# Kernel optimization log

Hardware: AMD Instinct MI355X
Metric: run time of the kernel (lower is better)

## Reference

```python
import jax, jax.numpy as jnp
import numpy as np

N_NODES = 50000
N_EDGES = 625000
D_IN, D_HID, D_OUT = 512, 128, 1


def gcn_conv(x, W, b, src, dst, n_nodes):
    """PyG GCNConv: add self-loops, symmetric D^-1/2 (A+I) D^-1/2 normalization.
    x: [N, d_in], W: [d_in, d_out], b: [d_out], src/dst: [E] int.
    """
    xw = x @ W  # [N, d_out] - linear before propagation (PyG order)
    # degree including self-loop
    deg = jax.ops.segment_sum(jnp.ones_like(src, dtype=xw.dtype), dst,
                              num_segments=n_nodes) + 1.0
    dinv = jax.lax.rsqrt(deg)  # [N]
    norm = dinv[src] * dinv[dst]  # [E]
    # neighbor aggregation (scatter-add over destination nodes)
    agg = jax.ops.segment_sum(xw[src] * norm[:, None], dst, num_segments=n_nodes)
    # self-loop contribution: norm_ii = dinv_i^2
    agg = agg + xw * (dinv * dinv)[:, None]
    return agg + b


def layer_norm(x, gamma, beta, eps=1e-5):
    mu = jnp.mean(x, axis=-1, keepdims=True)
    var = jnp.var(x, axis=-1, keepdims=True)
    return (x - mu) * jax.lax.rsqrt(var + eps) * gamma + beta


def setup_inputs() -> dict:
    key = jax.random.key(0)
    ks = jax.random.split(key, 12)
    x = jax.random.normal(ks[0], (N_NODES, D_IN), dtype=jnp.float32)
    edge_index = jax.random.randint(ks[1], (2, N_EDGES), 0, N_NODES, dtype=jnp.int64)

    def glorot(k, shape):
        lim = np.sqrt(6.0 / (shape[0] + shape[1]))
        return jax.random.uniform(k, shape, jnp.float32, -lim, lim)

    return {
        "x": x,
        "W1": glorot(ks[2], (D_IN, D_HID)), "b1": jnp.zeros((D_HID,), jnp.float32),
        "gamma1": jnp.ones((D_HID,), jnp.float32), "beta1": jnp.zeros((D_HID,), jnp.float32),
        "W2": glorot(ks[3], (D_HID, D_HID)), "b2": jnp.zeros((D_HID,), jnp.float32),
        "W3": glorot(ks[4], (D_HID, D_HID)), "b3": jnp.zeros((D_HID,), jnp.float32),
        "W4": glorot(ks[5], (D_HID, D_OUT)), "b4": jnp.zeros((D_OUT,), jnp.float32),
        "edge_index": edge_index,
    }


def reference(x, W1, b1, gamma1, beta1, W2, b2, W3, b3, W4, b4, edge_index):
    # eval mode: F.dropout(training=False) is identity
    src, dst = edge_index[0], edge_index[1]
    n = x.shape[0]
    h = jax.nn.relu(layer_norm(gcn_conv(x, W1, b1, src, dst, n), gamma1, beta1))
    h = jax.nn.relu(gcn_conv(h, W2, b2, src, dst, n))
    h = jax.nn.relu(gcn_conv(h, W3, b3, src, dst, n))
    h = gcn_conv(h, W4, b4, src, dst, n)
    return jnp.squeeze(h, axis=-1)  # [N]
```

## Files before the change

### kernel.cpp

```cpp
#include <hip/hip_runtime.h>
#include <hip/hip_bf16.h>
#include <cstdint>

#define D_IN 512
#define D_HID 128

typedef unsigned short u16;
typedef __attribute__((ext_vector_type(8))) short short8;
typedef __attribute__((ext_vector_type(4))) float f32x4;

__device__ __forceinline__ u16 f2bf(float f) {
    unsigned u = __float_as_uint(f);
    u = (u + 0x7FFFu + ((u >> 16) & 1u)) >> 16;
    return (u16)u;
}
__device__ __forceinline__ float bf_lo(unsigned u) { return __uint_as_float(u << 16); }
__device__ __forceinline__ float bf_hi(unsigned u) { return __uint_as_float(u & 0xFFFF0000u); }

__global__ __launch_bounds__(256) void k_deg_int(const int* __restrict__ dst,
                                                 int* __restrict__ deg, int E) {
    int e = blockIdx.x * 256 + threadIdx.x;
    if (e < E) atomicAdd(&deg[dst[e]], 1);
}

__global__ __launch_bounds__(256) void k_scan_block(const int* __restrict__ deg,
                                                    int* __restrict__ rowptr,
                                                    int* __restrict__ bsum, int N) {
    __shared__ int sh[256];
    int i = blockIdx.x * 256 + threadIdx.x;
    int v = (i < N) ? deg[i] : 0;
    sh[threadIdx.x] = v;
    __syncthreads();
#pragma unroll
    for (int off = 1; off < 256; off <<= 1) {
        int t = (threadIdx.x >= off) ? sh[threadIdx.x - off] : 0;
        __syncthreads();
        sh[threadIdx.x] += t;
        __syncthreads();
    }
    int incl = sh[threadIdx.x];
    if (i < N) rowptr[i] = incl - v;
    if (threadIdx.x == 255) bsum[blockIdx.x] = incl;
}

__global__ __launch_bounds__(256) void k_scan_partials(int* __restrict__ bsum, int P) {
    __shared__ int sh[256];
    int v = (threadIdx.x < P) ? bsum[threadIdx.x] : 0;
    sh[threadIdx.x] = v;
    __syncthreads();
#pragma unroll
    for (int off = 1; off < 256; off <<= 1) {
        int t = (threadIdx.x >= off) ? sh[threadIdx.x - off] : 0;
        __syncthreads();
        sh[threadIdx.x] += t;
        __syncthreads();
    }
    if (threadIdx.x < P) bsum[threadIdx.x] = sh[threadIdx.x] - v;
}

__global__ __launch_bounds__(256) void k_apply_offset(int* __restrict__ rowptr,
                                                      const int* __restrict__ bsum,
                                                      int* __restrict__ deg_cursor,
                                                      float* __restrict__ dinv,
                                                      int N, int E) {
    int i = blockIdx.x * 256 + threadIdx.x;
    if (i == 0) rowptr[N] = E;
    if (i >= N) return;
    int dv = deg_cursor[i];
    int rp = rowptr[i] + bsum[i >> 8];
    rowptr[i] = rp;
    deg_cursor[i] = rp;
    dinv[i] = rsqrtf((float)dv + 1.0f);
}

__global__ __launch_bounds__(256) void k_fill_csr(const int* __restrict__ src,
                                                  const int* __restrict__ dst,
                                                  int* __restrict__ cursor,
                                                  int* __restrict__ csr, int E) {
    int e = blockIdx.x * 256 + threadIdx.x;
    if (e >= E) return;
    int pos = atomicAdd(&cursor[dst[e]], 1);
    csr[pos] = src[e];
}

__global__ __launch_bounds__(256) void k_wt(const float* __restrict__ W,
                                            u16* __restrict__ WT, int K) {
    int t = blockIdx.x * 256 + threadIdx.x;
    if (t >= 128 * K) return;
    int c = t / K, k = t - c * K;
    WT[t] = f2bf(W[(size_t)k * 128 + c]);
}

template <int K>
__global__ __launch_bounds__(256) void k_gemm_mfma(const float* __restrict__ X,
                                                   const u16* __restrict__ WT,
                                                   u16* __restrict__ Y, int N) {
    __shared__ u16 Xs[64 * 40];
    __shared__ u16 Ws[128 * 40];
    const int tid = threadIdx.x;
    const int wv = tid >> 6;
    const int lane = tid & 63;
    const int row0 = blockIdx.x * 64;
    const int rsel = lane & 15;
    const int kgrp = (lane >> 4) * 8;

    f32x4 acc[8];
#pragma unroll
    for (int c = 0; c < 8; ++c) acc[c] = (f32x4){0.f, 0.f, 0.f, 0.f};

    for (int k0 = 0; k0 < K; k0 += 32) {
        {
            int r = tid >> 2;
            int kk = (tid & 3) * 8;
            int row = row0 + r;
            float v[8];
            if (row < N) {
                float4 p0 = *(const float4*)&X[(size_t)row * K + k0 + kk];
                float4 p1 = *(const float4*)&X[(size_t)row * K + k0 + kk + 4];
                v[0] = p0.x; v[1] = p0.y; v[2] = p0.z; v[3] = p0.w;
                v[4] = p1.x; v[5] = p1.y; v[6] = p1.z; v[7] = p1.w;
            } else {
#pragma unroll
                for (int i = 0; i < 8; ++i) v[i] = 0.f;
            }
            union { u16 us[8]; short8 v8; } tmp;
#pragma unroll
            for (int i = 0; i < 8; ++i) tmp.us[i] = f2bf(v[i]);
            *(short8*)&Xs[r * 40 + kk] = tmp.v8;
        }
        {
            int col = tid >> 1;
            int kh = (tid & 1) * 16;
            const u16* g = &WT[(size_t)col * K + k0 + kh];
            u16* d = &Ws[col * 40 + kh];
            *(short8*)d = *(const short8*)g;
            *(short8*)(d + 8) = *(const short8*)(g + 8);
        }
        __syncthreads();
        short8 a = *(const short8*)&Xs[(wv * 16 + rsel) * 40 + kgrp];
#pragma unroll
        for (int c = 0; c < 8; ++c) {
            short8 b = *(const short8*)&Ws[(c * 16 + rsel) * 40 + kgrp];
            acc[c] = __builtin_amdgcn_mfma_f32_16x16x32_bf16(a, b, acc[c], 0, 0, 0);
        }
        __syncthreads();
    }
#pragma unroll
    for (int r = 0; r < 4; ++r) {
        int row = row0 + wv * 16 + (lane >> 4) * 4 + r;
        if (row < N) {
#pragma unroll
            for (int c = 0; c < 8; ++c)
                Y[(size_t)row * 128 + c * 16 + rsel] = f2bf(acc[c][r]);
        }
    }
}

__global__ __launch_bounds__(256) void k_gather_ln_relu(const u16* __restrict__ XW,
                                                        const int* __restrict__ rowptr,
                                                        const int* __restrict__ csr,
                                                        const float* __restrict__ dinv,
                                                        const float* __restrict__ b,
                                                        const float* __restrict__ gamma,
                                                        const float* __restrict__ beta,
                                                        float* __restrict__ H, int N) {
    int node = blockIdx.x * 4 + (threadIdx.x >> 6);
    int lane = threadIdx.x & 63;
    if (node >= N) return;
    float di = dinv[node];
    int beg = rowptr[node], end = rowptr[node + 1];
    const int loff = 2 * lane;
    float a0 = 0.f, a1 = 0.f;
    int j = beg;
    for (; j + 3 < end; j += 4) {
        int s0 = csr[j], s1 = csr[j + 1], s2 = csr[j + 2], s3 = csr[j + 3];
        float w0 = dinv[s0], w1 = dinv[s1], w2 = dinv[s2], w3 = dinv[s3];
        unsigned u0 = *(const unsigned*)&XW[(size_t)s0 * 128 + loff];
        unsigned u1 = *(const unsigned*)&XW[(size_t)s1 * 128 + loff];
        unsigned u2 = *(const unsigned*)&XW[(size_t)s2 * 128 + loff];
        unsigned u3 = *(const unsigned*)&XW[(size_t)s3 * 128 + loff];
        a0 += bf_lo(u0) * w0 + bf_lo(u1) * w1 + bf_lo(u2) * w2 + bf_lo(u3) * w3;
        a1 += bf_hi(u0) * w0 + bf_hi(u1) * w1 + bf_hi(u2) * w2 + bf_hi(u3) * w3;
    }
    for (; j < end; ++j) {
        int s = csr[j];
        float w = dinv[s];
        unsigned u = *(const unsigned*)&XW[(size_t)s * 128 + loff];
        a0 += bf_lo(u) * w;
        a1 += bf_hi(u) * w;
    }
    unsigned us = *(const unsigned*)&XW[(size_t)node * 128 + loff];
    float d2 = di * di;
    float2 bb = *(const float2*)&b[loff];
    float v0 = a0 * di + bf_lo(us) * d2 + bb.x;
    float v1 = a1 * di + bf_hi(us) * d2 + bb.y;
    float s = v0 + v1;
    float sq = v0 * v0 + v1 * v1;
#pragma unroll
    for (int off = 32; off; off >>= 1) {
        s  += __shfl_xor(s, off);
        sq += __shfl_xor(sq, off);
    }
    float mu  = s * (1.f / 128.f);
    float var = sq * (1.f / 128.f) - mu * mu;
    float rr  = rsqrtf(var + 1e-5f);
    float2 gg = *(const float2*)&gamma[loff];
    float2 be = *(const float2*)&beta[loff];
    float o0 = fmaxf((v0 - mu) * rr * gg.x + be.x, 0.f);
    float o1 = fmaxf((v1 - mu) * rr * gg.y + be.y, 0.f);
    *(float2*)&H[(size_t)node * 128 + loff] = make_float2(o0, o1);
}

__global__ __launch_bounds__(256) void k_gather_relu(const u16* __restrict__ XW,
                                                     const int* __restrict__ rowptr,
                                                     const int* __restrict__ csr,
                                                     const float* __restrict__ dinv,
                                                     const float* __restrict__ b,
                                                     float* __restrict__ H, int N) {
    int node = blockIdx.x * 4 + (threadIdx.x >> 6);
    int lane = threadIdx.x & 63;
    if (node >= N) return;
    float di = dinv[node];
    int beg = rowptr[node], end = rowptr[node + 1];
    const int loff = 2 * lane;
    float a0 = 0.f, a1 = 0.f;
    int j = beg;
    for (; j + 3 < end; j += 4) {
        int s0 = csr[j], s1 = csr[j + 1], s2 = csr[j + 2], s3 = csr[j + 3];
        float w0 = dinv[s0], w1 = dinv[s1], w2 = dinv[s2], w3 = dinv[s3];
        unsigned u0 = *(const unsigned*)&XW[(size_t)s0 * 128 + loff];
        unsigned u1 = *(const unsigned*)&XW[(size_t)s1 * 128 + loff];
        unsigned u2 = *(const unsigned*)&XW[(size_t)s2 * 128 + loff];
        unsigned u3 = *(const unsigned*)&XW[(size_t)s3 * 128 + loff];
        a0 += bf_lo(u0) * w0 + bf_lo(u1) * w1 + bf_lo(u2) * w2 + bf_lo(u3) * w3;
        a1 += bf_hi(u0) * w0 + bf_hi(u1) * w1 + bf_hi(u2) * w2 + bf_hi(u3) * w3;
    }
    for (; j < end; ++j) {
        int s = csr[j];
        float w = dinv[s];
        unsigned u = *(const unsigned*)&XW[(size_t)s * 128 + loff];
        a0 += bf_lo(u) * w;
        a1 += bf_hi(u) * w;
    }
    unsigned us = *(const unsigned*)&XW[(size_t)node * 128 + loff];
    float d2 = di * di;
    float2 bb = *(const float2*)&b[loff];
    float v0 = fmaxf(a0 * di + bf_lo(us) * d2 + bb.x, 0.f);
    float v1 = fmaxf(a1 * di + bf_hi(us) * d2 + bb.y, 0.f);
    *(float2*)&H[(size_t)node * 128 + loff] = make_float2(v0, v1);
}

__global__ __launch_bounds__(256) void k_gather_dot(const u16* __restrict__ XW,
                                                    const int* __restrict__ rowptr,
                                                    const int* __restrict__ csr,
                                                    const float* __restrict__ dinv,
                                                    const float* __restrict__ b,
                                                    const float* __restrict__ W4,
                                                    float* __restrict__ XW4, int N) {
    int node = blockIdx.x * 4 + (threadIdx.x >> 6);
    int lane = threadIdx.x & 63;
    if (node >= N) return;
    float di = dinv[node];
    int beg = rowptr[node], end = rowptr[node + 1];
    const int loff = 2 * lane;
    float a0 = 0.f, a1 = 0.f;
    int j = beg;
    for (; j + 3 < end; j += 4) {
        int s0 = csr[j], s1 = csr[j + 1], s2 = csr[j + 2], s3 = csr[j + 3];
        float w0 = dinv[s0], w1 = dinv[s1], w2 = dinv[s2], w3 = dinv[s3];
        unsigned u0 = *(const unsigned*)&XW[(size_t)s0 * 128 + loff];
        unsigned u1 = *(const unsigned*)&XW[(size_t)s1 * 128 + loff];
        unsigned u2 = *(const unsigned*)&XW[(size_t)s2 * 128 + loff];
        unsigned u3 = *(const unsigned*)&XW[(size_t)s3 * 128 + loff];
        a0 += bf_lo(u0) * w0 + bf_lo(u1) * w1 + bf_lo(u2) * w2 + bf_lo(u3) * w3;
        a1 += bf_hi(u0) * w0 + bf_hi(u1) * w1 + bf_hi(u2) * w2 + bf_hi(u3) * w3;
    }
    for (; j < end; ++j) {
        int s = csr[j];
        float w = dinv[s];
        unsigned u = *(const unsigned*)&XW[(size_t)s * 128 + loff];
        a0 += bf_lo(u) * w;
        a1 += bf_hi(u) * w;
    }
    unsigned us = *(const unsigned*)&XW[(size_t)node * 128 + loff];
    float d2 = di * di;
    float2 bb = *(const float2*)&b[loff];
    float v0 = fmaxf(a0 * di + bf_lo(us) * d2 + bb.x, 0.f);
    float v1 = fmaxf(a1 * di + bf_hi(us) * d2 + bb.y, 0.f);
    float2 w4v = *(const float2*)&W4[loff];
    float t = v0 * w4v.x + v1 * w4v.y;
#pragma unroll
    for (int off = 32; off; off >>= 1) t += __shfl_xor(t, off);
    if (lane == 0) XW4[node] = t;
}

__global__ __launch_bounds__(256) void k_final_scalar(const float* __restrict__ XW4,
                                                      const int* __restrict__ rowptr,
                                                      const int* __restrict__ csr,
                                                      const float* __restrict__ dinv,
                                                      const float* __restrict__ b4,
                                                      float* __restrict__ OUT, int N) {
    int i = blockIdx.x * 256 + threadIdx.x;
    if (i >= N) return;
    float di = dinv[i];
    int beg = rowptr[i], end = rowptr[i + 1];
    float acc = 0.f;
    for (int j = beg; j < end; ++j) {
        int s = csr[j];
        acc += XW4[s] * dinv[s];
    }
    OUT[i] = acc * di + XW4[i] * di * di + b4[0];
}

static inline size_t alignup(size_t x) { return (x + 255) & ~(size_t)255; }

extern "C" void kernel_launch(void* const* d_in, const int* in_sizes, int n_in,
                              void* d_out, int out_size, void* d_ws, size_t ws_size,
                              hipStream_t stream) {
    const float* x      = (const float*)d_in[0];
    const float* W1     = (const float*)d_in[1];
    const float* b1     = (const float*)d_in[2];
    const float* gamma1 = (const float*)d_in[3];
    const float* beta1  = (const float*)d_in[4];
    const float* W2     = (const float*)d_in[5];
    const float* b2     = (const float*)d_in[6];
    const float* W3     = (const float*)d_in[7];
    const float* b3     = (const float*)d_in[8];
    const float* W4     = (const float*)d_in[9];
    const float* b4     = (const float*)d_in[10];
    const int*   ei     = (const int*)d_in[11];

    const int N = in_sizes[0] / D_IN;
    const int E = in_sizes[11] / 2;
    const int* src = ei;
    const int* dst = ei + E;

    char* ws = (char*)d_ws;
    size_t off = 0;
    int*   deg_cur = (int*)(ws + off);   off += alignup((size_t)N * 4);
    int*   rowptr  = (int*)(ws + off);   off += alignup((size_t)(N + 1) * 4);
    int*   bsum    = (int*)(ws + off);   off += alignup(256 * 4);
    float* dinv    = (float*)(ws + off); off += alignup((size_t)N * 4);
    float* xw4     = (float*)(ws + off); off += alignup((size_t)N * 4);
    int*   csr     = (int*)(ws + off);   off += alignup((size_t)E * 4);
    u16*   WT1     = (u16*)(ws + off);   off += alignup((size_t)128 * 512 * 2);
    u16*   WT2     = (u16*)(ws + off);   off += alignup((size_t)128 * 128 * 2);
    u16*   WT3     = (u16*)(ws + off);   off += alignup((size_t)128 * 128 * 2);
    u16*   XW      = (u16*)(ws + off);   off += alignup((size_t)N * 128 * 2);
    float* H       = (float*)(ws + off);

    const int scanBlocks = (N + 255) / 256;

    hipMemsetAsync(deg_cur, 0, (size_t)N * 4, stream);
    k_deg_int<<<(E + 255) / 256, 256, 0, stream>>>(dst, deg_cur, E);
    k_scan_block<<<scanBlocks, 256, 0, stream>>>(deg_cur, rowptr, bsum, N);
    k_scan_partials<<<1, 256, 0, stream>>>(bsum, scanBlocks);
    k_apply_offset<<<scanBlocks, 256, 0, stream>>>(rowptr, bsum, deg_cur, dinv, N, E);
    k_fill_csr<<<(E + 255) / 256, 256, 0, stream>>>(src, dst, deg_cur, csr, E);

    k_wt<<<(128 * 512 + 255) / 256, 256, 0, stream>>>(W1, WT1, 512);
    k_wt<<<(128 * 128 + 255) / 256, 256, 0, stream>>>(W2, WT2, 128);
    k_wt<<<(128 * 128 + 255) / 256, 256, 0, stream>>>(W3, WT3, 128);

    const int gemmGrid   = (N + 63) / 64;
    const int gatherGrid = (N + 3) / 4;

    k_gemm_mfma<512><<<gemmGrid, 256, 0, stream>>>(x, WT1, XW, N);
    k_gather_ln_relu<<<gatherGrid, 256, 0, stream>>>(XW, rowptr, csr, dinv,
                                                     b1, gamma1, beta1, H, N);
    k_gemm_mfma<128><<<gemmGrid, 256, 0, stream>>>(H, WT2, XW, N);
    k_gather_relu<<<gatherGrid, 256, 0, stream>>>(XW, rowptr, csr, dinv, b2, H, N);
    k_gemm_mfma<128><<<gemmGrid, 256, 0, stream>>>(H, WT3, XW, N);
    k_gather_dot<<<gatherGrid, 256, 0, stream>>>(XW, rowptr, csr, dinv, b3, W4, xw4, N);
    k_final_scalar<<<(N + 255) / 256, 256, 0, stream>>>(xw4, rowptr, csr, dinv,
                                                        b4, (float*)d_out, N);
}
```

Before: 399.0 us.

## Store hidden activations in bf16, widen gather loads, parallelize final aggregation

```diff
diff --git a/kernel.cpp b/kernel.cpp
--- a/kernel.cpp
+++ b/kernel.cpp
@@ -6,16 +6,18 @@
 #define D_HID 128
 
 typedef unsigned short u16;
+typedef unsigned int u32;
 typedef __attribute__((ext_vector_type(8))) short short8;
 typedef __attribute__((ext_vector_type(4))) float f32x4;
 
 __device__ __forceinline__ u16 f2bf(float f) {
-    unsigned u = __float_as_uint(f);
+    u32 u = __float_as_uint(f);
     u = (u + 0x7FFFu + ((u >> 16) & 1u)) >> 16;
     return (u16)u;
 }
-__device__ __forceinline__ float bf_lo(unsigned u) { return __uint_as_float(u << 16); }
-__device__ __forceinline__ float bf_hi(unsigned u) { return __uint_as_float(u & 0xFFFF0000u); }
+__device__ __forceinline__ float bfc(short x) {
+    return __uint_as_float(((u32)(u16)x) << 16);
+}
 
 __global__ __launch_bounds__(256) void k_deg_int(const int* __restrict__ dst,
                                                  int* __restrict__ deg, int E) {
@@ -83,16 +85,29 @@
     csr[pos] = src[e];
 }
 
-__global__ __launch_bounds__(256) void k_wt(const float* __restrict__ W,
-                                            u16* __restrict__ WT, int K) {
+__global__ __launch_bounds__(256) void k_wt_all(const float* __restrict__ W1,
+                                                const float* __restrict__ W2,
+                                                const float* __restrict__ W3,
+                                                u16* __restrict__ WT1,
+                                                u16* __restrict__ WT2,
+                                                u16* __restrict__ WT3) {
     int t = blockIdx.x * 256 + threadIdx.x;
-    if (t >= 128 * K) return;
-    int c = t / K, k = t - c * K;
-    WT[t] = f2bf(W[(size_t)k * 128 + c]);
-}
-
-template <int K>
-__global__ __launch_bounds__(256) void k_gemm_mfma(const float* __restrict__ X,
+    if (t < 65536) {
+        int c = t >> 9, k = t & 511;
+        WT1[t] = f2bf(W1[(size_t)k * 128 + c]);
+    } else if (t < 65536 + 16384) {
+        int u = t - 65536;
+        int c = u >> 7, k = u & 127;
+        WT2[u] = f2bf(W2[(size_t)k * 128 + c]);
+    } else if (t < 65536 + 32768) {
+        int u = t - 65536 - 16384;
+        int c = u >> 7, k = u & 127;
+        WT3[u] = f2bf(W3[(size_t)k * 128 + c]);
+    }
+}
+
+template <int K, typename TI>
+__global__ __launch_bounds__(256) void k_gemm_mfma(const TI* __restrict__ X,
                                                    const u16* __restrict__ WT,
                                                    u16* __restrict__ Y, int N) {
     __shared__ u16 Xs[64 * 40];
@@ -113,20 +128,26 @@
             int r = tid >> 2;
             int kk = (tid & 3) * 8;
             int row = row0 + r;
-            float v[8];
-            if (row < N) {
-                float4 p0 = *(const float4*)&X[(size_t)row * K + k0 + kk];
-                float4 p1 = *(const float4*)&X[(size_t)row * K + k0 + kk + 4];
-                v[0] = p0.x; v[1] = p0.y; v[2] = p0.z; v[3] = p0.w;
-                v[4] = p1.x; v[5] = p1.y; v[6] = p1.z; v[7] = p1.w;
+            if constexpr (sizeof(TI) == 4) {
+                float v[8];
+                if (row < N) {
+                    float4 p0 = *(const float4*)&X[(size_t)row * K + k0 + kk];
+                    float4 p1 = *(const float4*)&X[(size_t)row * K + k0 + kk + 4];
+                    v[0] = p0.x; v[1] = p0.y; v[2] = p0.z; v[3] = p0.w;
+                    v[4] = p1.x; v[5] = p1.y; v[6] = p1.z; v[7] = p1.w;
+                } else {
+#pragma unroll
+                    for (int i = 0; i < 8; ++i) v[i] = 0.f;
+                }
+                union { u16 us[8]; short8 v8; } tmp;
+#pragma unroll
+                for (int i = 0; i < 8; ++i) tmp.us[i] = f2bf(v[i]);
+                *(short8*)&Xs[r * 40 + kk] = tmp.v8;
             } else {
-#pragma unroll
-                for (int i = 0; i < 8; ++i) v[i] = 0.f;
+                short8 v8 = {};
+                if (row < N) v8 = *(const short8*)&X[(size_t)row * K + k0 + kk];
+                *(short8*)&Xs[r * 40 + kk] = v8;
             }
-            union { u16 us[8]; short8 v8; } tmp;
-#pragma unroll
-            for (int i = 0; i < 8; ++i) tmp.us[i] = f2bf(v[i]);
-            *(short8*)&Xs[r * 40 + kk] = tmp.v8;
         }
         {
             int col = tid >> 1;
@@ -156,6 +177,32 @@
     }
 }
 
+#define GATHER_CORE(XW, rowptr, csr, dinv, node, q, es, a)                         \
+    int beg = rowptr[node], end = rowptr[node + 1];                                \
+    float a[8];                                                                    \
+    _Pragma("unroll") for (int i = 0; i < 8; ++i) a[i] = 0.f;                      \
+    {                                                                              \
+        int j = beg + es;                                                          \
+        for (; j + 4 < end; j += 8) {                                              \
+            int s0 = csr[j], s1 = csr[j + 4];                                      \
+            float w0 = dinv[s0], w1 = dinv[s1];                                    \
+            short8 r0 = *(const short8*)&XW[(size_t)s0 * 128 + q * 8];             \
+            short8 r1 = *(const short8*)&XW[(size_t)s1 * 128 + q * 8];             \
+            _Pragma("unroll") for (int i = 0; i < 8; ++i)                          \
+                a[i] += bfc(r0[i]) * w0 + bfc(r1[i]) * w1;                         \
+        }                                                                          \
+        if (j < end) {                                                             \
+            int s = csr[j];                                                        \
+            float w = dinv[s];                                                     \
+            short8 r = *(const short8*)&XW[(size_t)s * 128 + q * 8];               \
+            _Pragma("unroll") for (int i = 0; i < 8; ++i) a[i] += bfc(r[i]) * w;   \
+        }                                                                          \
+    }                                                                              \
+    _Pragma("unroll") for (int i = 0; i < 8; ++i) {                                \
+        a[i] += __shfl_xor(a[i], 16);                                              \
+        a[i] += __shfl_xor(a[i], 32);                                              \
+    }
+
 __global__ __launch_bounds__(256) void k_gather_ln_relu(const u16* __restrict__ XW,
                                                         const int* __restrict__ rowptr,
                                                         const int* __restrict__ csr,
@@ -163,52 +210,49 @@
                                                         const float* __restrict__ b,
                                                         const float* __restrict__ gamma,
                                                         const float* __restrict__ beta,
-                                                        float* __restrict__ H, int N) {
+                                                        u16* __restrict__ H, int N) {
     int node = blockIdx.x * 4 + (threadIdx.x >> 6);
     int lane = threadIdx.x & 63;
+    int q = lane & 15;
+    int es = lane >> 4;
     if (node >= N) return;
     float di = dinv[node];
-    int beg = rowptr[node], end = rowptr[node + 1];
-    const int loff = 2 * lane;
-    float a0 = 0.f, a1 = 0.f;
-    int j = beg;
-    for (; j + 3 < end; j += 4) {
-        int s0 = csr[j], s1 = csr[j + 1], s2 = csr[j + 2], s3 = csr[j + 3];
-        float w0 = dinv[s0], w1 = dinv[s1], w2 = dinv[s2], w3 = dinv[s3];
-        unsigned u0 = *(const unsigned*)&XW[(size_t)s0 * 128 + loff];
-        unsigned u1 = *(const unsigned*)&XW[(size_t)s1 * 128 + loff];
-        unsigned u2 = *(const unsigned*)&XW[(size_t)s2 * 128 + loff];
-        unsigned u3 = *(const unsigned*)&XW[(size_t)s3 * 128 + loff];
-        a0 += bf_lo(u0) * w0 + bf_lo(u1) * w1 + bf_lo(u2) * w2 + bf_lo(u3) * w3;
-        a1 += bf_hi(u0) * w0 + bf_hi(u1) * w1 + bf_hi(u2) * w2 + bf_hi(u3) * w3;
-    }
-    for (; j < end; ++j) {
-        int s = csr[j];
-        float w = dinv[s];
-        unsigned u = *(const unsigned*)&XW[(size_t)s * 128 + loff];
-        a0 += bf_lo(u) * w;
-        a1 += bf_hi(u) * w;
-    }
-    unsigned us = *(const unsigned*)&XW[(size_t)node * 128 + loff];
+    GATHER_CORE(XW, rowptr, csr, dinv, node, q, es, a)
+    short8 us = *(const short8*)&XW[(size_t)node * 128 + q * 8];
     float d2 = di * di;
-    float2 bb = *(const float2*)&b[loff];
-    float v0 = a0 * di + bf_lo(us) * d2 + bb.x;
-    float v1 = a1 * di + bf_hi(us) * d2 + bb.y;
-    float s = v0 + v1;
-    float sq = v0 * v0 + v1 * v1;
-#pragma unroll
-    for (int off = 32; off; off >>= 1) {
+    float4 b0 = *(const float4*)&b[q * 8];
+    float4 b1 = *(const float4*)&b[q * 8 + 4];
+    float v[8];
+#pragma unroll
+    for (int i = 0; i < 8; ++i) {
+        float bb = (i < 4) ? ((const float*)&b0)[i] : ((const float*)&b1)[i - 4];
+        v[i] = a[i] * di + bfc(us[i]) * d2 + bb;
+    }
+    float s = 0.f, sq = 0.f;
+#pragma unroll
+    for (int i = 0; i < 8; ++i) { s += v[i]; sq += v[i] * v[i]; }
+#pragma unroll
+    for (int off = 8; off; off >>= 1) {
         s  += __shfl_xor(s, off);
         sq += __shfl_xor(sq, off);
     }
     float mu  = s * (1.f / 128.f);
     float var = sq * (1.f / 128.f) - mu * mu;
     float rr  = rsqrtf(var + 1e-5f);
-    float2 gg = *(const float2*)&gamma[loff];
-    float2 be = *(const float2*)&beta[loff];
-    float o0 = fmaxf((v0 - mu) * rr * gg.x + be.x, 0.f);
-    float o1 = fmaxf((v1 - mu) * rr * gg.y + be.y, 0.f);
-    *(float2*)&H[(size_t)node * 128 + loff] = make_float2(o0, o1);
+    float4 g0 = *(const float4*)&gamma[q * 8];
+    float4 g1 = *(const float4*)&gamma[q * 8 + 4];
+    float4 e0 = *(const float4*)&beta[q * 8];
+    float4 e1 = *(const float4*)&beta[q * 8 + 4];
+    if (es == 0) {
+        union { u16 us[8]; short8 v8; } o;
+#pragma unroll
+        for (int i = 0; i < 8; ++i) {
+            float gg = (i < 4) ? ((const float*)&g0)[i] : ((const float*)&g1)[i - 4];
+            float ee = (i < 4) ? ((const float*)&e0)[i] : ((const float*)&e1)[i - 4];
+            o.us[i] = f2bf(fmaxf((v[i] - mu) * rr * gg + ee, 0.f));
+        }
+        *(short8*)&H[(size_t)node * 128 + q * 8] = o.v8;
+    }
 }
 
 __global__ __launch_bounds__(256) void k_gather_relu(const u16* __restrict__ XW,
@@ -216,38 +260,26 @@
                                                      const int* __restrict__ csr,
                                                      const float* __restrict__ dinv,
                                                      const float* __restrict__ b,
-                                                     float* __restrict__ H, int N) {
+                                                     u16* __restrict__ H, int N) {
     int node = blockIdx.x * 4 + (threadIdx.x >> 6);
     int lane = threadIdx.x & 63;
+    int q = lane & 15;
+    int es = lane >> 4;
     if (node >= N) return;
     float di = dinv[node];
-    int beg = rowptr[node], end = rowptr[node + 1];
-    const int loff = 2 * lane;
-    float a0 = 0.f, a1 = 0.f;
-    int j = beg;
-    for (; j + 3 < end; j += 4) {
-        int s0 = csr[j], s1 = csr[j + 1], s2 = csr[j + 2], s3 = csr[j + 3];
-        float w0 = dinv[s0], w1 = dinv[s1], w2 = dinv[s2], w3 = dinv[s3];
-        unsigned u0 = *(const unsigned*)&XW[(size_t)s0 * 128 + loff];
-        unsigned u1 = *(const unsigned*)&XW[(size_t)s1 * 128 + loff];
-        unsigned u2 = *(const unsigned*)&XW[(size_t)s2 * 128 + loff];
-        unsigned u3 = *(const unsigned*)&XW[(size_t)s3 * 128 + loff];
-        a0 += bf_lo(u0) * w0 + bf_lo(u1) * w1 + bf_lo(u2) * w2 + bf_lo(u3) * w3;
-        a1 += bf_hi(u0) * w0 + bf_hi(u1) * w1 + bf_hi(u2) * w2 + bf_hi(u3) * w3;
-    }
-    for (; j < end; ++j) {
-        int s = csr[j];
-        float w = dinv[s];
-        unsigned u = *(const unsigned*)&XW[(size_t)s * 128 + loff];
-        a0 += bf_lo(u) * w;
-        a1 += bf_hi(u) * w;
-    }
-    unsigned us = *(const unsigned*)&XW[(size_t)node * 128 + loff];
+    GATHER_CORE(XW, rowptr, csr, dinv, node, q, es, a)
+    if (es != 0) return;
+    short8 us = *(const short8*)&XW[(size_t)node * 128 + q * 8];
     float d2 = di * di;
-    float2 bb = *(const float2*)&b[loff];
-    float v0 = fmaxf(a0 * di + bf_lo(us) * d2 + bb.x, 0.f);
-    float v1 = fmaxf(a1 * di + bf_hi(us) * d2 + bb.y, 0.f);
-    *(float2*)&H[(size_t)node * 128 + loff] = make_float2(v0, v1);
+    float4 b0 = *(const float4*)&b[q * 8];
+    float4 b1 = *(const float4*)&b[q * 8 + 4];
+    union { u16 us[8]; short8 v8; } o;
+#pragma unroll
+    for (int i = 0; i < 8; ++i) {
+        float bb = (i < 4) ? ((const float*)&b0)[i] : ((const float*)&b1)[i - 4];
+        o.us[i] = f2bf(fmaxf(a[i] * di + bfc(us[i]) * d2 + bb, 0.f));
+    }
+    *(short8*)&H[(size_t)node * 128 + q * 8] = o.v8;
 }
 
 __global__ __launch_bounds__(256) void k_gather_dot(const u16* __restrict__ XW,
@@ -259,38 +291,27 @@
                                                     float* __restrict__ XW4, int N) {
     int node = blockIdx.x * 4 + (threadIdx.x >> 6);
     int lane = threadIdx.x & 63;
+    int q = lane & 15;
+    int es = lane >> 4;
     if (node >= N) return;
     float di = dinv[node];
-    int beg = rowptr[node], end = rowptr[node + 1];
-    const int loff = 2 * lane;
-    float a0 = 0.f, a1 = 0.f;
-    int j = beg;
-    for (; j + 3 < end; j += 4) {
-        int s0 = csr[j], s1 = csr[j + 1], s2 = csr[j + 2], s3 = csr[j + 3];
-        float w0 = dinv[s0], w1 = dinv[s1], w2 = dinv[s2], w3 = dinv[s3];
-        unsigned u0 = *(const unsigned*)&XW[(size_t)s0 * 128 + loff];
-        unsigned u1 = *(const unsigned*)&XW[(size_t)s1 * 128 + loff];
-        unsigned u2 = *(const unsigned*)&XW[(size_t)s2 * 128 + loff];
-        unsigned u3 = *(const unsigned*)&XW[(size_t)s3 * 128 + loff];
-        a0 += bf_lo(u0) * w0 + bf_lo(u1) * w1 + bf_lo(u2) * w2 + bf_lo(u3) * w3;
-        a1 += bf_hi(u0) * w0 + bf_hi(u1) * w1 + bf_hi(u2) * w2 + bf_hi(u3) * w3;
-    }
-    for (; j < end; ++j) {
-        int s = csr[j];
-        float w = dinv[s];
-        unsigned u = *(const unsigned*)&XW[(size_t)s * 128 + loff];
-        a0 += bf_lo(u) * w;
-        a1 += bf_hi(u) * w;
-    }
-    unsigned us = *(const unsigned*)&XW[(size_t)node * 128 + loff];
+    GATHER_CORE(XW, rowptr, csr, dinv, node, q, es, a)
+    short8 us = *(const short8*)&XW[(size_t)node * 128 + q * 8];
     float d2 = di * di;
-    float2 bb = *(const float2*)&b[loff];
-    float v0 = fmaxf(a0 * di + bf_lo(us) * d2 + bb.x, 0.f);
-    float v1 = fmaxf(a1 * di + bf_hi(us) * d2 + bb.y, 0.f);
-    float2 w4v = *(const float2*)&W4[loff];
-    float t = v0 * w4v.x + v1 * w4v.y;
-#pragma unroll
-    for (int off = 32; off; off >>= 1) t += __shfl_xor(t, off);
+    float4 b0 = *(const float4*)&b[q * 8];
+    float4 b1 = *(const float4*)&b[q * 8 + 4];
+    float4 w0 = *(const float4*)&W4[q * 8];
+    float4 w1 = *(const float4*)&W4[q * 8 + 4];
+    float t = 0.f;
+#pragma unroll
+    for (int i = 0; i < 8; ++i) {
+        float bb = (i < 4) ? ((const float*)&b0)[i] : ((const float*)&b1)[i - 4];
+        float ww = (i < 4) ? ((const float*)&w0)[i] : ((const float*)&w1)[i - 4];
+        float v = fmaxf(a[i] * di + bfc(us[i]) * d2 + bb, 0.f);
+        t += v * ww;
+    }
+#pragma unroll
+    for (int off = 8; off; off >>= 1) t += __shfl_xor(t, off);
     if (lane == 0) XW4[node] = t;
 }
 
@@ -300,16 +321,21 @@
                                                       const float* __restrict__ dinv,
                                                       const float* __restrict__ b4,
                                                       float* __restrict__ OUT, int N) {
-    int i = blockIdx.x * 256 + threadIdx.x;
-    if (i >= N) return;
-    float di = dinv[i];
-    int beg = rowptr[i], end = rowptr[i + 1];
+    int node = blockIdx.x * 16 + (threadIdx.x >> 4);
+    int q = threadIdx.x & 15;
+    if (node >= N) return;
+    int beg = rowptr[node], end = rowptr[node + 1];
     float acc = 0.f;
-    for (int j = beg; j < end; ++j) {
+    for (int j = beg + q; j < end; j += 16) {
         int s = csr[j];
         acc += XW4[s] * dinv[s];
     }
-    OUT[i] = acc * di + XW4[i] * di * di + b4[0];
+#pragma unroll
+    for (int off = 8; off; off >>= 1) acc += __shfl_xor(acc, off);
+    if (q == 0) {
+        float di = dinv[node];
+        OUT[node] = acc * di + XW4[node] * di * di + b4[0];
+    }
 }
 
 static inline size_t alignup(size_t x) { return (x + 255) & ~(size_t)255; }
@@ -347,7 +373,7 @@
     u16*   WT2     = (u16*)(ws + off);   off += alignup((size_t)128 * 128 * 2);
     u16*   WT3     = (u16*)(ws + off);   off += alignup((size_t)128 * 128 * 2);
     u16*   XW      = (u16*)(ws + off);   off += alignup((size_t)N * 128 * 2);
-    float* H       = (float*)(ws + off);
+    u16*   H       = (u16*)(ws + off);
 
     const int scanBlocks = (N + 255) / 256;
 
@@ -358,20 +384,18 @@
     k_apply_offset<<<scanBlocks, 256, 0, stream>>>(rowptr, bsum, deg_cur, dinv, N, E);
     k_fill_csr<<<(E + 255) / 256, 256, 0, stream>>>(src, dst, deg_cur, csr, E);
 
-    k_wt<<<(128 * 512 + 255) / 256, 256, 0, stream>>>(W1, WT1, 512);
-    k_wt<<<(128 * 128 + 255) / 256, 256, 0, stream>>>(W2, WT2, 128);
-    k_wt<<<(128 * 128 + 255) / 256, 256, 0, stream>>>(W3, WT3, 128);
+    k_wt_all<<<(65536 + 32768 + 255) / 256, 256, 0, stream>>>(W1, W2, W3, WT1, WT2, WT3);
 
     const int gemmGrid   = (N + 63) / 64;
     const int gatherGrid = (N + 3) / 4;
 
-    k_gemm_mfma<512><<<gemmGrid, 256, 0, stream>>>(x, WT1, XW, N);
+    k_gemm_mfma<512, float><<<gemmGrid, 256, 0, stream>>>(x, WT1, XW, N);
     k_gather_ln_relu<<<gatherGrid, 256, 0, stream>>>(XW, rowptr, csr, dinv,
                                                      b1, gamma1, beta1, H, N);
-    k_gemm_mfma<128><<<gemmGrid, 256, 0, stream>>>(H, WT2, XW, N);
+    k_gemm_mfma<128, u16><<<gemmGrid, 256, 0, stream>>>(H, WT2, XW, N);
     k_gather_relu<<<gatherGrid, 256, 0, stream>>>(XW, rowptr, csr, dinv, b2, H, N);
-    k_gemm_mfma<128><<<gemmGrid, 256, 0, stream>>>(H, WT3, XW, N);
+    k_gemm_mfma<128, u16><<<gemmGrid, 256, 0, stream>>>(H, WT3, XW, N);
     k_gather_dot<<<gatherGrid, 256, 0, stream>>>(XW, rowptr, csr, dinv, b3, W4, xw4, N);
-    k_final_scalar<<<(N + 255) / 256, 256, 0, stream>>>(xw4, rowptr, csr, dinv,
-                                                        b4, (float*)d_out, N);
-}
+    k_final_scalar<<<(N + 15) / 16, 256, 0, stream>>>(xw4, rowptr, csr, dinv,
+                                                      b4, (float*)d_out, N);
+}
```

Result: faster. 375.4 us (-5.9%).
